# Kernel tuning notes

Measured on AMD Instinct MI355X. Metric: run time of the kernel, lower is better.

Reference implementation:

```python
import jax, jax.numpy as jnp
import numpy as np

N_QUBITS = 7
DEPTH = 2
DIM = 2 ** N_QUBITS  # 128
BATCH = 262144

# Qiskit little-endian convention: statevector index bit q = (idx >> q) & 1.
_idx = np.arange(DIM)
_bits = (_idx[:, None] >> np.arange(N_QUBITS)) & 1            # (DIM, N_QUBITS)
# CZ on all adjacent pairs (q, q+1): sign = (-1)^sum(bit_q * bit_{q+1})
_cz_parity = np.sum(_bits[:, :-1] * _bits[:, 1:], axis=1) % 2
CZ_PHASE = jnp.asarray(1.0 - 2.0 * _cz_parity, dtype=jnp.float32)   # (DIM,)
# Z_i expectation signs: <Z_i> = sum_idx p(idx) * (1 - 2*bit_i)
Z_SIGNS = jnp.asarray(1.0 - 2.0 * _bits, dtype=jnp.float32)         # (DIM, N_QUBITS)


def _apply_ry(state, q, theta_q):
    # state: (B, DIM) real amplitudes; RY is real so state stays real.
    lo = 2 ** q
    hi = DIM // (2 * lo)
    s = state.reshape(-1, hi, 2, lo)
    half = theta_q * 0.5
    c, sn = jnp.cos(half), jnp.sin(half)
    a0, a1 = s[:, :, 0, :], s[:, :, 1, :]
    out = jnp.stack([c * a0 - sn * a1, sn * a0 + c * a1], axis=2)
    return out.reshape(-1, DIM)


def setup_inputs() -> dict:
    key = jax.random.key(0)
    k1, k2 = jax.random.split(key)
    embed = jax.random.normal(k1, (BATCH, DIM), dtype=jnp.float32)
    theta = jax.random.normal(k2, (DEPTH * N_QUBITS,), dtype=jnp.float32) * 0.1
    return {"embed": embed, "theta": theta}


def reference(embed, theta):
    # Amplitude encoding: L2-normalize each row.
    state = embed / jnp.linalg.norm(embed, axis=1, keepdims=True)
    for d in range(DEPTH):
        for q in range(N_QUBITS):
            state = _apply_ry(state, q, theta[d * N_QUBITS + q])
        state = state * CZ_PHASE[None, :]
    probs = state * state                  # (B, DIM)
    return probs @ Z_SIGNS                 # (B, N_QUBITS)
```

## Files before the change

### kernel.cpp

```cpp
#include <hip/hip_runtime.h>
#include <utility>

#define NQ   7
#define DIM  128
#define HALF 64
#define RPB  32

template<class F, int... I>
__device__ __forceinline__ void static_for_impl(F&& f, std::integer_sequence<int, I...>) {
    (f(std::integral_constant<int, I>{}), ...);
}
template<int N, class F>
__device__ __forceinline__ void static_for(F&& f) {
    static_for_impl(static_cast<F&&>(f), std::make_integer_sequence<int, N>{});
}

__device__ __forceinline__ float swap_adj(float x) {
    int v = __builtin_amdgcn_update_dpp(0, __builtin_bit_cast(int, x),
                                        0xB1 ,
                                        0xF, 0xF, true);
    return __builtin_bit_cast(float, v);
}

__global__ __launch_bounds__(64, 2)
void qnat_kernel(const float* __restrict__ embed,
                 const float* __restrict__ theta,
                 float* __restrict__ out)
{
    __shared__ float4 tile[RPB * 33];
    const int lane = threadIdx.x;
    const int t = lane >> 1;
    const int h = lane & 1;
    const float4* __restrict__ g4 =
        reinterpret_cast<const float4*>(embed) + (size_t)blockIdx.x * (RPB * 32);

    static_for<16>([&](auto J) {
        constexpr int j = J.value;
        const float4 v = g4[j * 64 + lane];
        tile[(2 * j + (lane >> 5)) * 33 + (lane & 31)] = v;
    });
    __syncthreads();

    float st[HALF];
    static_for<16>([&](auto J) {
        constexpr int j = J.value;
        const float4 v = tile[t * 33 + h * 16 + j];
        st[4 * j + 0] = v.x;
        st[4 * j + 1] = v.y;
        st[4 * j + 2] = v.z;
        st[4 * j + 3] = v.w;
    });

    float ss = 0.f;
    static_for<HALF>([&](auto I) {
        constexpr int i = I.value;
        ss = fmaf(st[i], st[i], ss);
    });
    ss += swap_adj(ss);

    const float hs = h ? -1.f : 1.f;

    static_for<2>([&](auto D) {
        constexpr int d = D.value;
        static_for<6>([&](auto Q) {
            constexpr int q = Q.value;
            const float ha = 0.5f * theta[d * NQ + q];
            const float c_ = __cosf(ha), s_ = __sinf(ha);
            static_for<32>([&](auto P) {
                constexpr int p  = P.value;
                constexpr int lo = 1 << q;
                constexpr int i0 = ((p >> q) << (q + 1)) | (p & (lo - 1));
                constexpr int i1 = i0 | lo;
                const float a0 = st[i0], a1 = st[i1];
                st[i0] = fmaf(c_, a0, -s_ * a1);
                st[i1] = fmaf(s_, a0,  c_ * a1);
            });
        });
        {
            const float ha = 0.5f * theta[d * NQ + 6];
            const float c_ = __cosf(ha), s_ = __sinf(ha);
            const float sgn = h ? s_ : -s_;
            static_for<HALF>([&](auto J) {
                constexpr int j = J.value;
                const float other = swap_adj(st[j]);
                st[j] = fmaf(sgn, other, c_ * st[j]);
            });
        }
        static_for<HALF>([&](auto J) {
            constexpr int j = J.value;
            if constexpr ((__builtin_popcount(j & (j >> 1)) & 1) == 1) st[j] = -st[j];
            if constexpr (((j >> 5) & 1) == 1) st[j] *= hs;
        });
    });

    static_for<HALF>([&](auto J) {
        constexpr int j = J.value;
        st[j] *= st[j];
    });

    float o[NQ];
    static_for<6>([&](auto K) {
        constexpr int k = K.value;
        constexpr int n = HALF >> (k + 1);
        float acc = 0.f;
        static_for<32>([&](auto I) {
            constexpr int i = I.value;
            if constexpr (i < n) {
                const float a = st[2 * i], b = st[2 * i + 1];
                acc += a - b;
                st[i] = a + b;
            }
        });
        o[k] = acc;
    });
    static_for<6>([&](auto K) {
        constexpr int k = K.value;
        o[k] += swap_adj(o[k]);
    });
    {
        const float part = st[0];
        o[6] = hs * (part - swap_adj(part));
    }
    const float invss = __builtin_amdgcn_rcpf(ss);
    static_for<NQ>([&](auto K) { o[K.value] *= invss; });

    __syncthreads();
    float* ldsf = reinterpret_cast<float*>(tile);
    if (h == 0) {
        static_for<NQ>([&](auto K) {
            constexpr int k = K.value;
            ldsf[t * NQ + k] = o[k];
        });
    }
    __syncthreads();
    float* __restrict__ ob = out + (size_t)blockIdx.x * (RPB * NQ);
    static_for<4>([&](auto It) {
        constexpr int it = It.value;
        const int idx = it * 64 + lane;
        if constexpr (it < 3) {
            ob[idx] = ldsf[idx];
        } else {
            if (idx < RPB * NQ) ob[idx] = ldsf[idx];
        }
    });
}

extern "C" void kernel_launch(void* const* d_in, const int* in_sizes, int n_in,
                              void* d_out, int out_size, void* d_ws, size_t ws_size,
                              hipStream_t stream)
{
    const float* embed = (const float*)d_in[0];
    const float* theta = (const float*)d_in[1];
    float* out = (float*)d_out;
    const int batch = in_sizes[0] / DIM;
    dim3 grid(batch / RPB), block(64);
    hipLaunchKernelGGL(qnat_kernel, grid, block, 0, stream, embed, theta, out);
}
```

Before: 193.0 us.

## Load tiles via global_load_lds with XOR swizzle, hoist trig, derive norm from probabilities

Global loads now go straight into LDS through global_load_lds and use an XOR-swizzled layout in place of the padded tile. This removes the register round-trip and the padding while avoiding bank conflicts. The 14 cos/sin values are computed up front, overlapping with the async loads. The separate sum-of-squares pass is dropped: because the gates are orthogonal, the total probability after the circuit equals the input norm. The final CZ sign pass is skipped since squaring cancels it, and the Z-sign reduction is restructured to use S and T sums. The risk is a wrong swizzle mapping or async-load semantics, and a norm that is only equal up to float rounding.

```diff
diff --git a/kernel.cpp b/kernel.cpp
--- a/kernel.cpp
+++ b/kernel.cpp
@@ -27,36 +27,45 @@
                  const float* __restrict__ theta,
                  float* __restrict__ out)
 {
-    __shared__ float4 tile[RPB * 33];
+    __shared__ float4 tile[RPB * 32];
     const int lane = threadIdx.x;
     const int t = lane >> 1;
     const int h = lane & 1;
     const float4* __restrict__ g4 =
         reinterpret_cast<const float4*>(embed) + (size_t)blockIdx.x * (RPB * 32);
 
+    const int b5 = lane >> 5;
     static_for<16>([&](auto J) {
         constexpr int j = J.value;
-        const float4 v = g4[j * 64 + lane];
-        tile[(2 * j + (lane >> 5)) * 33 + (lane & 31)] = v;
+        const int m  = (2 * j + b5) & 7;
+        const int sf = 64 * j + (lane ^ m);
+        __builtin_amdgcn_global_load_lds(
+            (const __attribute__((address_space(1))) void*)(g4 + sf),
+            (__attribute__((address_space(3))) void*)(&tile[64 * j]),
+            16, 0, 0);
     });
+
+    float c_[2 * NQ], s_[2 * NQ];
+    static_for<2 * NQ>([&](auto G) {
+        constexpr int g = G.value;
+        const float ha = 0.5f * theta[g];
+        c_[g] = __cosf(ha);
+        s_[g] = __sinf(ha);
+    });
+
+    asm volatile("s_waitcnt vmcnt(0)" ::: "memory");
     __syncthreads();
 
     float st[HALF];
+    const int tl = t & 7;
     static_for<16>([&](auto J) {
         constexpr int j = J.value;
-        const float4 v = tile[t * 33 + h * 16 + j];
+        const float4 v = tile[t * 32 + h * 16 + (j ^ tl)];
         st[4 * j + 0] = v.x;
         st[4 * j + 1] = v.y;
         st[4 * j + 2] = v.z;
         st[4 * j + 3] = v.w;
     });
-
-    float ss = 0.f;
-    static_for<HALF>([&](auto I) {
-        constexpr int i = I.value;
-        ss = fmaf(st[i], st[i], ss);
-    });
-    ss += swap_adj(ss);
 
     const float hs = h ? -1.f : 1.f;
 
@@ -64,33 +73,33 @@
         constexpr int d = D.value;
         static_for<6>([&](auto Q) {
             constexpr int q = Q.value;
-            const float ha = 0.5f * theta[d * NQ + q];
-            const float c_ = __cosf(ha), s_ = __sinf(ha);
+            const float cc = c_[d * NQ + q], sn = s_[d * NQ + q];
             static_for<32>([&](auto P) {
                 constexpr int p  = P.value;
                 constexpr int lo = 1 << q;
                 constexpr int i0 = ((p >> q) << (q + 1)) | (p & (lo - 1));
                 constexpr int i1 = i0 | lo;
                 const float a0 = st[i0], a1 = st[i1];
-                st[i0] = fmaf(c_, a0, -s_ * a1);
-                st[i1] = fmaf(s_, a0,  c_ * a1);
+                st[i0] = fmaf(cc, a0, -sn * a1);
+                st[i1] = fmaf(sn, a0,  cc * a1);
             });
         });
         {
-            const float ha = 0.5f * theta[d * NQ + 6];
-            const float c_ = __cosf(ha), s_ = __sinf(ha);
-            const float sgn = h ? s_ : -s_;
+            const float cc = c_[d * NQ + 6], sn = s_[d * NQ + 6];
+            const float sgn = h ? sn : -sn;
             static_for<HALF>([&](auto J) {
                 constexpr int j = J.value;
                 const float other = swap_adj(st[j]);
-                st[j] = fmaf(sgn, other, c_ * st[j]);
+                st[j] = fmaf(sgn, other, cc * st[j]);
             });
         }
-        static_for<HALF>([&](auto J) {
-            constexpr int j = J.value;
-            if constexpr ((__builtin_popcount(j & (j >> 1)) & 1) == 1) st[j] = -st[j];
-            if constexpr (((j >> 5) & 1) == 1) st[j] *= hs;
-        });
+        if constexpr (d == 0) {
+            static_for<HALF>([&](auto J) {
+                constexpr int j = J.value;
+                if constexpr ((__builtin_popcount(j & (j >> 1)) & 1) == 1) st[j] = -st[j];
+                if constexpr (((j >> 5) & 1) == 1) st[j] *= hs;
+            });
+        }
     });
 
     static_for<HALF>([&](auto J) {
@@ -99,29 +108,36 @@
     });
 
     float o[NQ];
-    static_for<6>([&](auto K) {
-        constexpr int k = K.value;
+    float Se = 0.f, So = 0.f;
+    static_for<32>([&](auto I) {
+        constexpr int i = I.value;
+        const float a = st[2 * i], b = st[2 * i + 1];
+        Se += a; So += b;
+        st[i] = a + b;
+    });
+    o[0] = Se - So;
+    const float T = Se + So;
+    static_for<5>([&](auto K) {
+        constexpr int k = K.value + 1;
         constexpr int n = HALF >> (k + 1);
-        float acc = 0.f;
-        static_for<32>([&](auto I) {
+        float S = 0.f;
+        static_for<16>([&](auto I) {
             constexpr int i = I.value;
             if constexpr (i < n) {
                 const float a = st[2 * i], b = st[2 * i + 1];
-                acc += a - b;
+                S += a;
                 st[i] = a + b;
             }
         });
-        o[k] = acc;
+        o[k] = fmaf(2.f, S, -T);
     });
     static_for<6>([&](auto K) {
         constexpr int k = K.value;
         o[k] += swap_adj(o[k]);
     });
-    {
-        const float part = st[0];
-        o[6] = hs * (part - swap_adj(part));
-    }
-    const float invss = __builtin_amdgcn_rcpf(ss);
+    const float Tsw = swap_adj(T);
+    o[6] = hs * (T - Tsw);
+    const float invss = __builtin_amdgcn_rcpf(T + Tsw);
     static_for<NQ>([&](auto K) { o[K.value] *= invss; });
 
     __syncthreads();
```

After: 194.6 us. About the same (+0.8%).
